# Performance work log

Measured on AMD Instinct MI355X. Metric: run time of the kernel, lower is better.

## Reference

```python
import jax, jax.numpy as jnp
import numpy as np

IN, OUT, S = 4096, 4096, 256
B, T = 4, 2048

# Straight-through-estimator sign quantizer (binary quant of low-rank factors).
@jax.custom_vjp
def ste_sign(x):
    return jnp.sign(x)

def _ste_fwd(x):
    return jnp.sign(x), None

def _ste_bwd(_, g):
    return (g,)

ste_sign.defvjp(_ste_fwd, _ste_bwd)


def setup_inputs() -> dict:
    key = jax.random.key(0)
    ks = jax.random.split(key, 14)
    nrm = lambda k, shp, s: jax.random.normal(k, shp, dtype=jnp.float32) * s
    uni = lambda k, shp: jax.random.uniform(k, shp, dtype=jnp.float32, minval=0.1, maxval=1.0)
    return {
        "x": nrm(ks[0], (B, T, IN), 1.0),
        "V": nrm(ks[1], (S, IN), 0.02),
        "U": nrm(ks[2], (OUT, S), 0.02),
        "v1": uni(ks[3], (1, S)),
        "v2": uni(ks[4], (1, IN)),
        "u1": uni(ks[5], (1, OUT)),
        "u2": uni(ks[6], (1, S)),
        "V_R": nrm(ks[7], (S, IN), 0.02),
        "U_R": nrm(ks[8], (OUT, S), 0.02),
        "v1_R": uni(ks[9], (1, S)),
        "v2_R": uni(ks[10], (1, IN)),
        "u1_R": uni(ks[11], (1, OUT)),
        "u2_R": uni(ks[12], (1, S)),
        "bias": nrm(ks[13], (OUT,), 0.02),
    }


def _branch(x2, V, U, v1, v2, u1, u2):
    # y = (((x * v2) @ sign(V).T) * (v1*u2)) @ sign(U).T * u1   (left-to-right, as in torch)
    Vq = ste_sign(V)          # [S, IN]
    Uq = ste_sign(U)          # [OUT, S]
    h = (x2 * v2) @ Vq.T      # [N, S]
    h = h * (v1 * u2)         # per-rank scale
    y = h @ Uq.T              # [N, OUT]
    return y * u1


def reference(x, V, U, v1, v2, u1, u2, V_R, U_R, v1_R, v2_R, u1_R, u2_R, bias):
    shp = x.shape
    x2 = x.reshape(-1, shp[-1])                                  # [N, IN]
    y = _branch(x2, V, U, v1, v2, u1, u2)
    y = y + _branch(x2, V_R, U_R, v1_R, v2_R, u1_R, u2_R)        # residual low-rank branch
    y = y + bias
    return y.reshape(shp[:-1] + (OUT,))
```

## Files before the change

### kernel.cpp

```cpp
#include <hip/hip_runtime.h>
#include <hip/hip_bf16.h>
#include <stdint.h>
#include <stddef.h>

typedef __attribute__((ext_vector_type(8))) short short8;
typedef __attribute__((ext_vector_type(4))) float floatx4;

#define AS_GLOBAL(p) (const __attribute__((address_space(1))) void*)(p)
#define AS_LDS(p)    (__attribute__((address_space(3))) void*)(p)

static constexpr int IN_DIM  = 4096;
static constexpr int OUT_DIM = 4096;
static constexpr int S_DIM   = 256;
static constexpr int S2      = 512;

__global__ void prep_kernel(const float* __restrict__ V, const float* __restrict__ v2,
                            const float* __restrict__ V_R, const float* __restrict__ v2_R,
                            const float* __restrict__ U, const float* __restrict__ u1,
                            const float* __restrict__ v1, const float* __restrict__ u2,
                            const float* __restrict__ U_R, const float* __restrict__ u1_R,
                            const float* __restrict__ v1_R, const float* __restrict__ u2_R,
                            const float* __restrict__ x,
                            __hip_bfloat16* __restrict__ W1,
                            __hip_bfloat16* __restrict__ W2,
                            __hip_bfloat16* __restrict__ Xb) {
  const int bid = blockIdx.x;
  if (bid < 2048) {
    const int idx4 = (bid * 256 + threadIdx.x) * 4;
    const int i = idx4 & (IN_DIM - 1);
    const int s = idx4 >> 12;
    floatx4 w, sc;
    if (s < S_DIM) {
      w  = *(const floatx4*)(V + s * IN_DIM + i);
      sc = *(const floatx4*)(v2 + i);
    } else {
      w  = *(const floatx4*)(V_R + (s - S_DIM) * IN_DIM + i);
      sc = *(const floatx4*)(v2_R + i);
    }
    union { ushort4 v; __hip_bfloat16 h[4]; } u;
#pragma unroll
    for (int j = 0; j < 4; ++j) {
      const float sg = (w[j] > 0.f) ? 1.f : ((w[j] < 0.f) ? -1.f : 0.f);
      u.h[j] = __float2bfloat16(sg * sc[j]);
    }
    *(ushort4*)((unsigned short*)W1 + idx4) = u.v;
  } else if (bid < 4096) {
    const int idx4 = ((bid - 2048) * 256 + threadIdx.x) * 4;
    const int s = idx4 & (S2 - 1);
    const int o = idx4 >> 9;
    floatx4 w, scs;
    float sco;
    if (s < S_DIM) {
      w   = *(const floatx4*)(U + o * S_DIM + s);
      sco = u1[o];
      const floatx4 a = *(const floatx4*)(v1 + s);
      const floatx4 b = *(const floatx4*)(u2 + s);
      scs = a * b;
    } else {
      const int ss = s - S_DIM;
      w   = *(const floatx4*)(U_R + o * S_DIM + ss);
      sco = u1_R[o];
      const floatx4 a = *(const floatx4*)(v1_R + ss);
      const floatx4 b = *(const floatx4*)(u2_R + ss);
      scs = a * b;
    }
    union { ushort4 v; __hip_bfloat16 h[4]; } u;
#pragma unroll
    for (int j = 0; j < 4; ++j) {
      const float sg = (w[j] > 0.f) ? 1.f : ((w[j] < 0.f) ? -1.f : 0.f);
      u.h[j] = __float2bfloat16(sg * sco * scs[j]);
    }
    *(ushort4*)((unsigned short*)W2 + idx4) = u.v;
  } else {
    const int idx = (bid - 4096) * 256 + threadIdx.x;
    const floatx4 f0 = *((const floatx4*)x + idx * 2);
    const floatx4 f1 = *((const floatx4*)x + idx * 2 + 1);
    union { short8 v; __hip_bfloat16 h[8]; } u;
    u.h[0] = __float2bfloat16(f0.x); u.h[1] = __float2bfloat16(f0.y);
    u.h[2] = __float2bfloat16(f0.z); u.h[3] = __float2bfloat16(f0.w);
    u.h[4] = __float2bfloat16(f1.x); u.h[5] = __float2bfloat16(f1.y);
    u.h[6] = __float2bfloat16(f1.z); u.h[7] = __float2bfloat16(f1.w);
    *((short8*)Xb + idx) = u.v;
  }
}

__global__ __launch_bounds__(256, 2)
void gemm1_kernel(const __hip_bfloat16* __restrict__ A,
                  const __hip_bfloat16* __restrict__ B,
                  __hip_bfloat16* __restrict__ C) {
  constexpr int K = IN_DIM;
  constexpr int N = S2;
  constexpr int BM = 128, BN = 64, BK = 64;

  __shared__ __hip_bfloat16 As[2][BM * BK];
  __shared__ __hip_bfloat16 Bs[2][BN * BK];

  const int t = threadIdx.x;
  const int wave = t >> 6;
  const int lane = t & 63;
  const int r16 = lane & 15;
  const int quad = lane >> 4;

  const int f = blockIdx.x;
  const int c = f & 7;
  const int l = f >> 3;
  const int tm0 = (c * 8 + (l >> 3)) * BM;
  const int tn0 = (l & 7) * BN;

  const int wm = (wave & 1) * 64;
  const int wn = (wave >> 1) * 32;

  floatx4 acc[4][2] = {};

  const int pa_row = t >> 3;
  const int pa_ql0 = (t & 7);
  const int pb_row = t >> 3;

  auto stage = [&](int buf, int k0) {
#pragma unroll
    for (int i = 0; i < 4; ++i) {
      const int p = t + i * 256;
      const int row = p >> 3;
      const int ql = (p & 7) ^ (row & 7);
      const __hip_bfloat16* gp = A + (size_t)(tm0 + row) * K + k0 + ql * 8;
      __builtin_amdgcn_global_load_lds(AS_GLOBAL(gp), AS_LDS((char*)&As[buf][0] + p * 16), 16, 0, 0);
    }
#pragma unroll
    for (int i = 0; i < 2; ++i) {
      const int p = t + i * 256;
      const int row = p >> 3;
      const int ql = (p & 7) ^ (row & 7);
      const __hip_bfloat16* gp = B + (size_t)(tn0 + row) * K + k0 + ql * 8;
      __builtin_amdgcn_global_load_lds(AS_GLOBAL(gp), AS_LDS((char*)&Bs[buf][0] + p * 16), 16, 0, 0);
    }
  };

  stage(0, 0);
  __syncthreads();

  int buf = 0;
  for (int k0 = 0; k0 < K; k0 += BK) {
    if (k0 + BK < K) stage(buf ^ 1, k0 + BK);

    const char* as = (const char*)&As[buf][0];
    const char* bs = (const char*)&Bs[buf][0];
#pragma unroll
    for (int ks = 0; ks < 2; ++ks) {
      short8 a[4], b[2];
      const int cc = ks * 4 + quad;
#pragma unroll
      for (int i = 0; i < 4; ++i) {
        const int ar = wm + i * 16 + r16;
        a[i] = *reinterpret_cast<const short8*>(as + (ar * 8 + (cc ^ (ar & 7))) * 16);
      }
#pragma unroll
      for (int j = 0; j < 2; ++j) {
        const int br = wn + j * 16 + r16;
        b[j] = *reinterpret_cast<const short8*>(bs + (br * 8 + (cc ^ (br & 7))) * 16);
      }
#pragma unroll
      for (int i = 0; i < 4; ++i)
#pragma unroll
        for (int j = 0; j < 2; ++j)
          acc[i][j] = __builtin_amdgcn_mfma_f32_16x16x32_bf16(a[i], b[j], acc[i][j], 0, 0, 0);
    }
    __syncthreads();
    buf ^= 1;
  }

#pragma unroll
  for (int i = 0; i < 4; ++i)
#pragma unroll
    for (int j = 0; j < 2; ++j)
#pragma unroll
      for (int r = 0; r < 4; ++r) {
        const int row = tm0 + wm + i * 16 + quad * 4 + r;
        const int col = tn0 + wn + j * 16 + r16;
        C[(size_t)row * N + col] = __float2bfloat16(acc[i][j][r]);
      }
}

__global__ __launch_bounds__(256, 3)
void gemm2_kernel(const __hip_bfloat16* __restrict__ A,
                  const __hip_bfloat16* __restrict__ B,
                  const float* __restrict__ bias,
                  float* __restrict__ C) {
  constexpr int K = S2;
  constexpr int N = OUT_DIM;
  constexpr int BM = 128, BN = 128, BK = 64;

  __shared__ __hip_bfloat16 As[BM * BK];
  __shared__ __hip_bfloat16 Bs[BN * BK];

  const int t = threadIdx.x;
  const int wave = t >> 6;
  const int lane = t & 63;
  const int r16 = lane & 15;
  const int quad = lane >> 4;

  const int f = blockIdx.x;
  const int c = f & 7;
  const int l = f >> 3;
  const int tm0 = (c * 8 + (l >> 5)) * BM;
  const int tn0 = (l & 31) * BN;

  const int wm = (wave & 1) * 64;
  const int wn = (wave >> 1) * 64;

  floatx4 acc[4][4] = {};

  for (int k0 = 0; k0 < K; k0 += BK) {
#pragma unroll
    for (int i = 0; i < 4; ++i) {
      const int p = t + i * 256;
      const int row = p >> 3;
      const int ql = (p & 7) ^ (row & 7);
      const __hip_bfloat16* gp = A + (size_t)(tm0 + row) * K + k0 + ql * 8;
      __builtin_amdgcn_global_load_lds(AS_GLOBAL(gp), AS_LDS((char*)As + p * 16), 16, 0, 0);
    }
#pragma unroll
    for (int i = 0; i < 4; ++i) {
      const int p = t + i * 256;
      const int row = p >> 3;
      const int ql = (p & 7) ^ (row & 7);
      const __hip_bfloat16* gp = B + (size_t)(tn0 + row) * K + k0 + ql * 8;
      __builtin_amdgcn_global_load_lds(AS_GLOBAL(gp), AS_LDS((char*)Bs + p * 16), 16, 0, 0);
    }
    __syncthreads();

#pragma unroll
    for (int ks = 0; ks < 2; ++ks) {
      short8 a[4], b[4];
      const int cc = ks * 4 + quad;
#pragma unroll
      for (int i = 0; i < 4; ++i) {
        const int ar = wm + i * 16 + r16;
        a[i] = *reinterpret_cast<const short8*>((const char*)As + (ar * 8 + (cc ^ (ar & 7))) * 16);
      }
#pragma unroll
      for (int j = 0; j < 4; ++j) {
        const int br = wn + j * 16 + r16;
        b[j] = *reinterpret_cast<const short8*>((const char*)Bs + (br * 8 + (cc ^ (br & 7))) * 16);
      }
#pragma unroll
      for (int i = 0; i < 4; ++i)
#pragma unroll
        for (int j = 0; j < 4; ++j)
          acc[i][j] = __builtin_amdgcn_mfma_f32_16x16x32_bf16(a[i], b[j], acc[i][j], 0, 0, 0);
    }
    __syncthreads();
  }

  float bi[4];
#pragma unroll
  for (int j = 0; j < 4; ++j) bi[j] = bias[tn0 + wn + j * 16 + r16];

#pragma unroll
  for (int i = 0; i < 4; ++i)
#pragma unroll
    for (int j = 0; j < 4; ++j)
#pragma unroll
      for (int r = 0; r < 4; ++r) {
        const int row = tm0 + wm + i * 16 + quad * 4 + r;
        const int col = tn0 + wn + j * 16 + r16;
        C[(size_t)row * N + col] = acc[i][j][r] + bi[j];
      }
}

extern "C" void kernel_launch(void* const* d_in, const int* in_sizes, int n_in,
                              void* d_out, int out_size, void* d_ws, size_t ws_size,
                              hipStream_t stream) {
  const float* x    = (const float*)d_in[0];
  const float* V    = (const float*)d_in[1];
  const float* U    = (const float*)d_in[2];
  const float* v1   = (const float*)d_in[3];
  const float* v2   = (const float*)d_in[4];
  const float* u1   = (const float*)d_in[5];
  const float* u2   = (const float*)d_in[6];
  const float* V_R  = (const float*)d_in[7];
  const float* U_R  = (const float*)d_in[8];
  const float* v1_R = (const float*)d_in[9];
  const float* v2_R = (const float*)d_in[10];
  const float* u1_R = (const float*)d_in[11];
  const float* u2_R = (const float*)d_in[12];
  const float* bias = (const float*)d_in[13];
  float* out = (float*)d_out;

  const int M = in_sizes[0] / IN_DIM;

  char* ws = (char*)d_ws;
  __hip_bfloat16* W1 = (__hip_bfloat16*)ws;
  __hip_bfloat16* W2 = (__hip_bfloat16*)(ws + (size_t)4 * 1024 * 1024);
  __hip_bfloat16* H  = (__hip_bfloat16*)(ws + (size_t)8 * 1024 * 1024);
  __hip_bfloat16* Xb = (__hip_bfloat16*)(ws + (size_t)16 * 1024 * 1024);

  const int cvt_blocks = (M * IN_DIM) / (8 * 256);
  prep_kernel<<<4096 + cvt_blocks, 256, 0, stream>>>(
      V, v2, V_R, v2_R, U, u1, v1, u2, U_R, u1_R, v1_R, u2_R, x, W1, W2, Xb);

  gemm1_kernel<<<(M / 128) * (S2 / 64), 256, 0, stream>>>(Xb, W1, H);

  gemm2_kernel<<<(M / 128) * (OUT_DIM / 128), 256, 0, stream>>>(H, W2, bias, out);
}
```

Baseline: 345.8 us.

## Retile gemm1 to 64x128 two-wave blocks and double-buffer gemm2 LDS

```diff
diff --git a/kernel.cpp b/kernel.cpp
--- a/kernel.cpp
+++ b/kernel.cpp
@@ -84,13 +84,13 @@
   }
 }
 
-__global__ __launch_bounds__(256, 2)
+__global__ __launch_bounds__(128)
 void gemm1_kernel(const __hip_bfloat16* __restrict__ A,
                   const __hip_bfloat16* __restrict__ B,
                   __hip_bfloat16* __restrict__ C) {
   constexpr int K = IN_DIM;
   constexpr int N = S2;
-  constexpr int BM = 128, BN = 64, BK = 64;
+  constexpr int BM = 64, BN = 128, BK = 64;
 
   __shared__ __hip_bfloat16 As[2][BM * BK];
   __shared__ __hip_bfloat16 Bs[2][BN * BK];
@@ -104,30 +104,24 @@
   const int f = blockIdx.x;
   const int c = f & 7;
   const int l = f >> 3;
-  const int tm0 = (c * 8 + (l >> 3)) * BM;
-  const int tn0 = (l & 7) * BN;
-
-  const int wm = (wave & 1) * 64;
-  const int wn = (wave >> 1) * 32;
-
-  floatx4 acc[4][2] = {};
-
-  const int pa_row = t >> 3;
-  const int pa_ql0 = (t & 7);
-  const int pb_row = t >> 3;
+  const int tm0 = (c * 16 + (l >> 2)) * BM;
+  const int tn0 = (l & 3) * BN;
+  const int wn = wave * 64;
+
+  floatx4 acc[4][4] = {};
 
   auto stage = [&](int buf, int k0) {
 #pragma unroll
     for (int i = 0; i < 4; ++i) {
-      const int p = t + i * 256;
+      const int p = t + i * 128;
       const int row = p >> 3;
       const int ql = (p & 7) ^ (row & 7);
       const __hip_bfloat16* gp = A + (size_t)(tm0 + row) * K + k0 + ql * 8;
       __builtin_amdgcn_global_load_lds(AS_GLOBAL(gp), AS_LDS((char*)&As[buf][0] + p * 16), 16, 0, 0);
     }
 #pragma unroll
-    for (int i = 0; i < 2; ++i) {
-      const int p = t + i * 256;
+    for (int i = 0; i < 8; ++i) {
+      const int p = t + i * 128;
       const int row = p >> 3;
       const int ql = (p & 7) ^ (row & 7);
       const __hip_bfloat16* gp = B + (size_t)(tn0 + row) * K + k0 + ql * 8;
@@ -146,22 +140,22 @@
     const char* bs = (const char*)&Bs[buf][0];
 #pragma unroll
     for (int ks = 0; ks < 2; ++ks) {
-      short8 a[4], b[2];
+      short8 a[4], b[4];
       const int cc = ks * 4 + quad;
 #pragma unroll
       for (int i = 0; i < 4; ++i) {
-        const int ar = wm + i * 16 + r16;
+        const int ar = i * 16 + r16;
         a[i] = *reinterpret_cast<const short8*>(as + (ar * 8 + (cc ^ (ar & 7))) * 16);
       }
 #pragma unroll
-      for (int j = 0; j < 2; ++j) {
+      for (int j = 0; j < 4; ++j) {
         const int br = wn + j * 16 + r16;
         b[j] = *reinterpret_cast<const short8*>(bs + (br * 8 + (cc ^ (br & 7))) * 16);
       }
 #pragma unroll
       for (int i = 0; i < 4; ++i)
 #pragma unroll
-        for (int j = 0; j < 2; ++j)
+        for (int j = 0; j < 4; ++j)
           acc[i][j] = __builtin_amdgcn_mfma_f32_16x16x32_bf16(a[i], b[j], acc[i][j], 0, 0, 0);
     }
     __syncthreads();
@@ -171,16 +165,16 @@
 #pragma unroll
   for (int i = 0; i < 4; ++i)
 #pragma unroll
-    for (int j = 0; j < 2; ++j)
+    for (int j = 0; j < 4; ++j)
 #pragma unroll
       for (int r = 0; r < 4; ++r) {
-        const int row = tm0 + wm + i * 16 + quad * 4 + r;
+        const int row = tm0 + i * 16 + quad * 4 + r;
         const int col = tn0 + wn + j * 16 + r16;
         C[(size_t)row * N + col] = __float2bfloat16(acc[i][j][r]);
       }
 }
 
-__global__ __launch_bounds__(256, 3)
+__global__ __launch_bounds__(256, 2)
 void gemm2_kernel(const __hip_bfloat16* __restrict__ A,
                   const __hip_bfloat16* __restrict__ B,
                   const float* __restrict__ bias,
@@ -189,8 +183,8 @@
   constexpr int N = OUT_DIM;
   constexpr int BM = 128, BN = 128, BK = 64;
 
-  __shared__ __hip_bfloat16 As[BM * BK];
-  __shared__ __hip_bfloat16 Bs[BN * BK];
+  __shared__ __hip_bfloat16 As[2][BM * BK];
+  __shared__ __hip_bfloat16 Bs[2][BN * BK];
 
   const int t = threadIdx.x;
   const int wave = t >> 6;
@@ -209,14 +203,14 @@
 
   floatx4 acc[4][4] = {};
 
-  for (int k0 = 0; k0 < K; k0 += BK) {
+  auto stage = [&](int buf, int k0) {
 #pragma unroll
     for (int i = 0; i < 4; ++i) {
       const int p = t + i * 256;
       const int row = p >> 3;
       const int ql = (p & 7) ^ (row & 7);
       const __hip_bfloat16* gp = A + (size_t)(tm0 + row) * K + k0 + ql * 8;
-      __builtin_amdgcn_global_load_lds(AS_GLOBAL(gp), AS_LDS((char*)As + p * 16), 16, 0, 0);
+      __builtin_amdgcn_global_load_lds(AS_GLOBAL(gp), AS_LDS((char*)&As[buf][0] + p * 16), 16, 0, 0);
     }
 #pragma unroll
     for (int i = 0; i < 4; ++i) {
@@ -224,10 +218,19 @@
       const int row = p >> 3;
       const int ql = (p & 7) ^ (row & 7);
       const __hip_bfloat16* gp = B + (size_t)(tn0 + row) * K + k0 + ql * 8;
-      __builtin_amdgcn_global_load_lds(AS_GLOBAL(gp), AS_LDS((char*)Bs + p * 16), 16, 0, 0);
-    }
-    __syncthreads();
-
+      __builtin_amdgcn_global_load_lds(AS_GLOBAL(gp), AS_LDS((char*)&Bs[buf][0] + p * 16), 16, 0, 0);
+    }
+  };
+
+  stage(0, 0);
+  __syncthreads();
+
+  int buf = 0;
+  for (int k0 = 0; k0 < K; k0 += BK) {
+    if (k0 + BK < K) stage(buf ^ 1, k0 + BK);
+
+    const char* as = (const char*)&As[buf][0];
+    const char* bs = (const char*)&Bs[buf][0];
 #pragma unroll
     for (int ks = 0; ks < 2; ++ks) {
       short8 a[4], b[4];
@@ -235,12 +238,12 @@
 #pragma unroll
       for (int i = 0; i < 4; ++i) {
         const int ar = wm + i * 16 + r16;
-        a[i] = *reinterpret_cast<const short8*>((const char*)As + (ar * 8 + (cc ^ (ar & 7))) * 16);
+        a[i] = *reinterpret_cast<const short8*>(as + (ar * 8 + (cc ^ (ar & 7))) * 16);
       }
 #pragma unroll
       for (int j = 0; j < 4; ++j) {
         const int br = wn + j * 16 + r16;
-        b[j] = *reinterpret_cast<const short8*>((const char*)Bs + (br * 8 + (cc ^ (br & 7))) * 16);
+        b[j] = *reinterpret_cast<const short8*>(bs + (br * 8 + (cc ^ (br & 7))) * 16);
       }
 #pragma unroll
       for (int i = 0; i < 4; ++i)
@@ -249,6 +252,7 @@
           acc[i][j] = __builtin_amdgcn_mfma_f32_16x16x32_bf16(a[i], b[j], acc[i][j], 0, 0, 0);
     }
     __syncthreads();
+    buf ^= 1;
   }
 
   float bi[4];
@@ -298,7 +302,7 @@
   prep_kernel<<<4096 + cvt_blocks, 256, 0, stream>>>(
       V, v2, V_R, v2_R, U, u1, v1, u2, U_R, u1_R, v1_R, u2_R, x, W1, W2, Xb);
 
-  gemm1_kernel<<<(M / 128) * (S2 / 64), 256, 0, stream>>>(Xb, W1, H);
+  gemm1_kernel<<<(M / 64) * (S2 / 128), 128, 0, stream>>>(Xb, W1, H);
 
   gemm2_kernel<<<(M / 128) * (OUT_DIM / 128), 256, 0, stream>>>(H, W2, bias, out);
 }
```

Result: slower. 356.7 us (+3.2%).

## Fuse fp32-to-bf16 conversion of x into gemm1 A-tile loading

Applied to the files above, without the earlier changes.

```diff
diff --git a/kernel.cpp b/kernel.cpp
--- a/kernel.cpp
+++ b/kernel.cpp
@@ -20,10 +20,8 @@
                             const float* __restrict__ v1, const float* __restrict__ u2,
                             const float* __restrict__ U_R, const float* __restrict__ u1_R,
                             const float* __restrict__ v1_R, const float* __restrict__ u2_R,
-                            const float* __restrict__ x,
                             __hip_bfloat16* __restrict__ W1,
-                            __hip_bfloat16* __restrict__ W2,
-                            __hip_bfloat16* __restrict__ Xb) {
+                            __hip_bfloat16* __restrict__ W2) {
   const int bid = blockIdx.x;
   if (bid < 2048) {
     const int idx4 = (bid * 256 + threadIdx.x) * 4;
@@ -44,7 +42,7 @@
       u.h[j] = __float2bfloat16(sg * sc[j]);
     }
     *(ushort4*)((unsigned short*)W1 + idx4) = u.v;
-  } else if (bid < 4096) {
+  } else {
     const int idx4 = ((bid - 2048) * 256 + threadIdx.x) * 4;
     const int s = idx4 & (S2 - 1);
     const int o = idx4 >> 9;
@@ -71,21 +69,11 @@
       u.h[j] = __float2bfloat16(sg * sco * scs[j]);
     }
     *(ushort4*)((unsigned short*)W2 + idx4) = u.v;
-  } else {
-    const int idx = (bid - 4096) * 256 + threadIdx.x;
-    const floatx4 f0 = *((const floatx4*)x + idx * 2);
-    const floatx4 f1 = *((const floatx4*)x + idx * 2 + 1);
-    union { short8 v; __hip_bfloat16 h[8]; } u;
-    u.h[0] = __float2bfloat16(f0.x); u.h[1] = __float2bfloat16(f0.y);
-    u.h[2] = __float2bfloat16(f0.z); u.h[3] = __float2bfloat16(f0.w);
-    u.h[4] = __float2bfloat16(f1.x); u.h[5] = __float2bfloat16(f1.y);
-    u.h[6] = __float2bfloat16(f1.z); u.h[7] = __float2bfloat16(f1.w);
-    *((short8*)Xb + idx) = u.v;
   }
 }
 
 __global__ __launch_bounds__(256, 2)
-void gemm1_kernel(const __hip_bfloat16* __restrict__ A,
+void gemm1_kernel(const float* __restrict__ X,
                   const __hip_bfloat16* __restrict__ B,
                   __hip_bfloat16* __restrict__ C) {
   constexpr int K = IN_DIM;
@@ -112,19 +100,32 @@
 
   floatx4 acc[4][2] = {};
 
-  const int pa_row = t >> 3;
-  const int pa_ql0 = (t & 7);
-  const int pb_row = t >> 3;
-
-  auto stage = [&](int buf, int k0) {
+  floatx4 areg[4][2];
+
+  auto loadA = [&](int k0) {
 #pragma unroll
     for (int i = 0; i < 4; ++i) {
       const int p = t + i * 256;
       const int row = p >> 3;
       const int ql = (p & 7) ^ (row & 7);
-      const __hip_bfloat16* gp = A + (size_t)(tm0 + row) * K + k0 + ql * 8;
-      __builtin_amdgcn_global_load_lds(AS_GLOBAL(gp), AS_LDS((char*)&As[buf][0] + p * 16), 16, 0, 0);
-    }
+      const float* gp = X + (size_t)(tm0 + row) * K + k0 + ql * 8;
+      areg[i][0] = *(const floatx4*)gp;
+      areg[i][1] = *(const floatx4*)(gp + 4);
+    }
+  };
+  auto writeA = [&](int buf) {
+#pragma unroll
+    for (int i = 0; i < 4; ++i) {
+      const int p = t + i * 256;
+      union { short8 v; __hip_bfloat16 h[8]; } u;
+#pragma unroll
+      for (int j = 0; j < 4; ++j) u.h[j]     = __float2bfloat16(areg[i][0][j]);
+#pragma unroll
+      for (int j = 0; j < 4; ++j) u.h[4 + j] = __float2bfloat16(areg[i][1][j]);
+      *reinterpret_cast<short8*>((char*)&As[buf][0] + p * 16) = u.v;
+    }
+  };
+  auto stageB = [&](int buf, int k0) {
 #pragma unroll
     for (int i = 0; i < 2; ++i) {
       const int p = t + i * 256;
@@ -135,12 +136,15 @@
     }
   };
 
-  stage(0, 0);
+  loadA(0);
+  stageB(0, 0);
+  writeA(0);
   __syncthreads();
 
   int buf = 0;
   for (int k0 = 0; k0 < K; k0 += BK) {
-    if (k0 + BK < K) stage(buf ^ 1, k0 + BK);
+    const bool next = (k0 + BK < K);
+    if (next) { loadA(k0 + BK); stageB(buf ^ 1, k0 + BK); }
 
     const char* as = (const char*)&As[buf][0];
     const char* bs = (const char*)&Bs[buf][0];
@@ -164,6 +168,8 @@
         for (int j = 0; j < 2; ++j)
           acc[i][j] = __builtin_amdgcn_mfma_f32_16x16x32_bf16(a[i], b[j], acc[i][j], 0, 0, 0);
     }
+
+    if (next) writeA(buf ^ 1);
     __syncthreads();
     buf ^= 1;
   }
@@ -292,13 +298,11 @@
   __hip_bfloat16* W1 = (__hip_bfloat16*)ws;
   __hip_bfloat16* W2 = (__hip_bfloat16*)(ws + (size_t)4 * 1024 * 1024);
   __hip_bfloat16* H  = (__hip_bfloat16*)(ws + (size_t)8 * 1024 * 1024);
-  __hip_bfloat16* Xb = (__hip_bfloat16*)(ws + (size_t)16 * 1024 * 1024);
-
-  const int cvt_blocks = (M * IN_DIM) / (8 * 256);
-  prep_kernel<<<4096 + cvt_blocks, 256, 0, stream>>>(
-      V, v2, V_R, v2_R, U, u1, v1, u2, U_R, u1_R, v1_R, u2_R, x, W1, W2, Xb);
-
-  gemm1_kernel<<<(M / 128) * (S2 / 64), 256, 0, stream>>>(Xb, W1, H);
+
+  prep_kernel<<<4096, 256, 0, stream>>>(
+      V, v2, V_R, v2_R, U, u1, v1, u2, U_R, u1_R, v1_R, u2_R, W1, W2);
+
+  gemm1_kernel<<<(M / 128) * (S2 / 64), 256, 0, stream>>>(x, W1, H);
 
   gemm2_kernel<<<(M / 128) * (OUT_DIM / 128), 256, 0, stream>>>(H, W2, bias, out);
 }
```

After: 363.0 us. 5.0% more time.

## Keep two tiles in flight with explicit vmcnt waits in both GEMMs

Applied to the files above, without the earlier changes.

```diff
diff --git a/kernel.cpp b/kernel.cpp
--- a/kernel.cpp
+++ b/kernel.cpp
@@ -8,6 +8,10 @@
 
 #define AS_GLOBAL(p) (const __attribute__((address_space(1))) void*)(p)
 #define AS_LDS(p)    (__attribute__((address_space(3))) void*)(p)
+
+#define WAIT_VM6() asm volatile("s_waitcnt vmcnt(6)" ::: "memory")
+#define WAIT_VM8() asm volatile("s_waitcnt vmcnt(8)" ::: "memory")
+#define WAIT_VM0() asm volatile("s_waitcnt vmcnt(0)" ::: "memory")
 
 static constexpr int IN_DIM  = 4096;
 static constexpr int OUT_DIM = 4096;
@@ -91,6 +95,7 @@
   constexpr int K = IN_DIM;
   constexpr int N = S2;
   constexpr int BM = 128, BN = 64, BK = 64;
+  constexpr int NT = K / BK;
 
   __shared__ __hip_bfloat16 As[2][BM * BK];
   __shared__ __hip_bfloat16 Bs[2][BN * BK];
@@ -111,10 +116,6 @@
   const int wn = (wave >> 1) * 32;
 
   floatx4 acc[4][2] = {};
-
-  const int pa_row = t >> 3;
-  const int pa_ql0 = (t & 7);
-  const int pb_row = t >> 3;
 
   auto stage = [&](int buf, int k0) {
 #pragma unroll
@@ -136,12 +137,14 @@
   };
 
   stage(0, 0);
-  __syncthreads();
-
-  int buf = 0;
-  for (int k0 = 0; k0 < K; k0 += BK) {
-    if (k0 + BK < K) stage(buf ^ 1, k0 + BK);
-
+  stage(1, BK);
+
+  for (int ti = 0; ti < NT; ++ti) {
+    if (ti < NT - 1) { WAIT_VM6(); } else { WAIT_VM0(); }
+    __builtin_amdgcn_sched_barrier(0);
+    __builtin_amdgcn_s_barrier();
+
+    const int buf = ti & 1;
     const char* as = (const char*)&As[buf][0];
     const char* bs = (const char*)&Bs[buf][0];
 #pragma unroll
@@ -164,8 +167,9 @@
         for (int j = 0; j < 2; ++j)
           acc[i][j] = __builtin_amdgcn_mfma_f32_16x16x32_bf16(a[i], b[j], acc[i][j], 0, 0, 0);
     }
-    __syncthreads();
-    buf ^= 1;
+
+    __builtin_amdgcn_s_barrier();
+    if (ti + 2 < NT) stage(buf, (ti + 2) * BK);
   }
 
 #pragma unroll
@@ -180,7 +184,7 @@
       }
 }
 
-__global__ __launch_bounds__(256, 3)
+__global__ __launch_bounds__(256, 2)
 void gemm2_kernel(const __hip_bfloat16* __restrict__ A,
                   const __hip_bfloat16* __restrict__ B,
                   const float* __restrict__ bias,
@@ -188,9 +192,10 @@
   constexpr int K = S2;
   constexpr int N = OUT_DIM;
   constexpr int BM = 128, BN = 128, BK = 64;
-
-  __shared__ __hip_bfloat16 As[BM * BK];
-  __shared__ __hip_bfloat16 Bs[BN * BK];
+  constexpr int NT = K / BK;
+
+  __shared__ __hip_bfloat16 As[2][BM * BK];
+  __shared__ __hip_bfloat16 Bs[2][BN * BK];
 
   const int t = threadIdx.x;
   const int wave = t >> 6;
@@ -209,14 +214,14 @@
 
   floatx4 acc[4][4] = {};
 
-  for (int k0 = 0; k0 < K; k0 += BK) {
+  auto stage = [&](int buf, int k0) {
 #pragma unroll
     for (int i = 0; i < 4; ++i) {
       const int p = t + i * 256;
       const int row = p >> 3;
       const int ql = (p & 7) ^ (row & 7);
       const __hip_bfloat16* gp = A + (size_t)(tm0 + row) * K + k0 + ql * 8;
-      __builtin_amdgcn_global_load_lds(AS_GLOBAL(gp), AS_LDS((char*)As + p * 16), 16, 0, 0);
+      __builtin_amdgcn_global_load_lds(AS_GLOBAL(gp), AS_LDS((char*)&As[buf][0] + p * 16), 16, 0, 0);
     }
 #pragma unroll
     for (int i = 0; i < 4; ++i) {
@@ -224,10 +229,21 @@
       const int row = p >> 3;
       const int ql = (p & 7) ^ (row & 7);
       const __hip_bfloat16* gp = B + (size_t)(tn0 + row) * K + k0 + ql * 8;
-      __builtin_amdgcn_global_load_lds(AS_GLOBAL(gp), AS_LDS((char*)Bs + p * 16), 16, 0, 0);
-    }
-    __syncthreads();
-
+      __builtin_amdgcn_global_load_lds(AS_GLOBAL(gp), AS_LDS((char*)&Bs[buf][0] + p * 16), 16, 0, 0);
+    }
+  };
+
+  stage(0, 0);
+  stage(1, BK);
+
+  for (int ti = 0; ti < NT; ++ti) {
+    if (ti < NT - 1) { WAIT_VM8(); } else { WAIT_VM0(); }
+    __builtin_amdgcn_sched_barrier(0);
+    __builtin_amdgcn_s_barrier();
+
+    const int buf = ti & 1;
+    const char* as = (const char*)&As[buf][0];
+    const char* bs = (const char*)&Bs[buf][0];
 #pragma unroll
     for (int ks = 0; ks < 2; ++ks) {
       short8 a[4], b[4];
@@ -235,12 +251,12 @@
 #pragma unroll
       for (int i = 0; i < 4; ++i) {
         const int ar = wm + i * 16 + r16;
-        a[i] = *reinterpret_cast<const short8*>((const char*)As + (ar * 8 + (cc ^ (ar & 7))) * 16);
+        a[i] = *reinterpret_cast<const short8*>(as + (ar * 8 + (cc ^ (ar & 7))) * 16);
       }
 #pragma unroll
       for (int j = 0; j < 4; ++j) {
         const int br = wn + j * 16 + r16;
-        b[j] = *reinterpret_cast<const short8*>((const char*)Bs + (br * 8 + (cc ^ (br & 7))) * 16);
+        b[j] = *reinterpret_cast<const short8*>(bs + (br * 8 + (cc ^ (br & 7))) * 16);
       }
 #pragma unroll
       for (int i = 0; i < 4; ++i)
@@ -248,7 +264,9 @@
         for (int j = 0; j < 4; ++j)
           acc[i][j] = __builtin_amdgcn_mfma_f32_16x16x32_bf16(a[i], b[j], acc[i][j], 0, 0, 0);
     }
-    __syncthreads();
+
+    __builtin_amdgcn_s_barrier();
+    if (ti + 2 < NT) stage(buf, (ti + 2) * BK);
   }
 
   float bi[4];
```

Result: no change. 346.9 us (+0.3%).
